# Kernel tuning notes

Hardware: AMD Instinct MI355X
Metric: run time of the kernel (lower is better)

The kernel has to match this reference:

```python
import jax, jax.numpy as jnp
import numpy as np

B = 1048576
INPUT_DIM = 64
NUM_LAYERS = 8   # number of trees
DEPTH = 6
TREE_DIM = 2
NUM_LEAVES = 2 ** DEPTH


def setup_inputs() -> dict:
    key = jax.random.key(0)
    ks = jax.random.split(key, 6)
    x = jax.random.normal(ks[0], (B, INPUT_DIM), dtype=jnp.float32)
    # Stacked per-tree, per-level Linear(input_dim, 1) selectors.
    W_sel = jax.random.normal(ks[1], (NUM_LAYERS, DEPTH, INPUT_DIM), dtype=jnp.float32) / np.sqrt(INPUT_DIM)
    b_sel = jax.random.normal(ks[2], (NUM_LAYERS, DEPTH), dtype=jnp.float32) * 0.01
    leaf_values = jax.random.normal(ks[3], (NUM_LAYERS, NUM_LEAVES, TREE_DIM), dtype=jnp.float32)
    fc_w = jax.random.normal(ks[4], (2, NUM_LAYERS * TREE_DIM), dtype=jnp.float32) / np.sqrt(NUM_LAYERS * TREE_DIM)
    fc_b = jax.random.normal(ks[5], (2,), dtype=jnp.float32) * 0.01
    return {"x": x, "W_sel": W_sel, "b_sel": b_sel, "leaf_values": leaf_values,
            "fc_w": fc_w, "fc_b": fc_b}


def reference(x, W_sel, b_sel, leaf_values, fc_w, fc_b):
    # All trees / levels in one contraction: [B, T, D]
    logits = jnp.einsum('bi,tdi->btd', x, W_sel) + b_sel
    # sigmoid(z) > 0.5  <=>  z > 0, but keep explicit sigmoid for faithfulness
    bits = (jax.nn.sigmoid(logits) > 0.5).astype(jnp.int32)  # [B, T, D]
    # leaf_indices = fold(idx*2 + bit) == sum bit_l * 2^(D-1-l)
    powers = (2 ** jnp.arange(DEPTH - 1, -1, -1)).astype(jnp.int32)  # [D]
    leaf_idx = jnp.sum(bits * powers, axis=-1)  # [B, T]
    # Per-tree leaf gather: leaf_values[t, leaf_idx[b, t]] -> [B, T, C]
    tree_ids = jnp.arange(NUM_LAYERS)[None, :]  # [1, T]
    leaves = leaf_values[tree_ids, leaf_idx]    # [B, T, C]
    concatenated = leaves.reshape(x.shape[0], NUM_LAYERS * TREE_DIM)
    return concatenated @ fc_w.T + fc_b
```

## Files before the change

kernel.cpp:

```cpp
#include <hip/hip_runtime.h>
#include <stdint.h>


typedef float f32x2 __attribute__((ext_vector_type(2)));
typedef float f32x4 __attribute__((ext_vector_type(4)));

static constexpr int   kBlocks = 4096;
static constexpr float kTau    = 1.5f * 0x1p-24f;
static constexpr float kMargin = 1e-4f;

__device__ __noinline__ float np_exact_dot(const float* __restrict__ xs,
                                           const float* __restrict__ w) {
#pragma clang fp contract(off)
  float s[4];
#pragma unroll
  for (int L = 0; L < 4; ++L) {
    float t = xs[12 + L] * w[12 + L];
    t = xs[8 + L] * w[8 + L] + t;
    t = xs[4 + L] * w[4 + L] + t;
    t = xs[0 + L] * w[0 + L] + t;
#pragma unroll
    for (int j = 1; j < 4; ++j) {
      const int o = 16 * j;
      t = xs[o + 12 + L] * w[o + 12 + L] + t;
      t = xs[o +  8 + L] * w[o +  8 + L] + t;
      t = xs[o +  4 + L] * w[o +  4 + L] + t;
      t = xs[o +  0 + L] * w[o +  0 + L] + t;
    }
    s[L] = t;
  }
  return (s[0] + s[1]) + (s[2] + s[3]);
}

__global__ __launch_bounds__(256) void forest_fast(
    const float* __restrict__ x,
    const float* __restrict__ Wsel,
    const float* __restrict__ bsel,
    const float* __restrict__ leaf,
    const float* __restrict__ fcw,
    const float* __restrict__ fcb,
    float* __restrict__ out)
{
  __shared__ f32x2 lleaf[512];
  ((f32x4*)lleaf)[threadIdx.x] = ((const f32x4*)leaf)[threadIdx.x];
  __syncthreads();

  const int lane = threadIdx.x & 63;
  const int wave = threadIdx.x >> 6;
  const int row  = (blockIdx.x * 4 + wave) * 64 + lane;
  const float* __restrict__ xrow = x + (size_t)row * 64;

  f32x2 xr2[32];
  {
    const f32x4* xp = (const f32x4*)xrow;
#pragma unroll
    for (int q = 0; q < 16; ++q) {
      const f32x4 v = xp[q];
      f32x2 h0; h0.x = v.x; h0.y = v.y;
      f32x2 h1; h1.x = v.z; h1.y = v.w;
      xr2[2 * q]     = h0;
      xr2[2 * q + 1] = h1;
    }
  }

  uint64_t bits = 0, flag = 0;
#pragma unroll 4
  for (int d = 0; d < 48; ++d) {
    const f32x2* __restrict__ w2 = (const f32x2*)(Wsel + d * 64);
    f32x2 c0 = {0.f, 0.f}, c1 = {0.f, 0.f}, c2 = {0.f, 0.f}, c3 = {0.f, 0.f};
#pragma unroll
    for (int i = 0; i < 8; ++i) {
      c0 = __builtin_elementwise_fma(xr2[4 * i + 0], w2[4 * i + 0], c0);
      c1 = __builtin_elementwise_fma(xr2[4 * i + 1], w2[4 * i + 1], c1);
      c2 = __builtin_elementwise_fma(xr2[4 * i + 2], w2[4 * i + 2], c2);
      c3 = __builtin_elementwise_fma(xr2[4 * i + 3], w2[4 * i + 3], c3);
    }
    const f32x2 s = (c0 + c1) + (c2 + c3);
    const float z = (s.x + s.y) + bsel[d];
    bits |= (uint64_t)(z > kTau ? 1u : 0u) << d;
    flag |= (uint64_t)(__builtin_fabsf(z - kTau) < kMargin ? 1u : 0u) << d;
  }

  while (flag) {
    const int d = __builtin_ctzll(flag);
    flag &= flag - 1;
    const float z = np_exact_dot(xrow, Wsel + d * 64) + bsel[d];
    const uint64_t m = 1ull << d;
    bits = (z > kTau) ? (bits | m) : (bits & ~m);
  }

  float o0 = fcb[0], o1 = fcb[1];
#pragma unroll
  for (int t = 0; t < 8; ++t) {
    int idx = 0;
#pragma unroll
    for (int l = 0; l < 6; ++l)
      idx = idx * 2 + (int)((bits >> (t * 6 + l)) & 1u);
    const f32x2 lv = lleaf[t * 64 + idx];
    o0 = fmaf(lv.x, fcw[2 * t], o0);
    o0 = fmaf(lv.y, fcw[2 * t + 1], o0);
    o1 = fmaf(lv.x, fcw[16 + 2 * t], o1);
    o1 = fmaf(lv.y, fcw[16 + 2 * t + 1], o1);
  }
  f32x2 r; r.x = o0; r.y = o1;
  ((f32x2*)out)[row] = r;
}

extern "C" void kernel_launch(void* const* d_in, const int* in_sizes, int n_in,
                              void* d_out, int out_size, void* d_ws, size_t ws_size,
                              hipStream_t stream) {
  (void)in_sizes; (void)n_in; (void)out_size; (void)d_ws; (void)ws_size;
  forest_fast<<<kBlocks, 256, 0, stream>>>(
      (const float*)d_in[0],
      (const float*)d_in[1],
      (const float*)d_in[2],
      (const float*)d_in[3],
      (const float*)d_in[4],
      (const float*)d_in[5],
      (float*)d_out);
}
```

Baseline: 394.6 us.

## Compute selector logits with split-bf16 MFMA instead of scalar FP32 FMAs

Replaces the per-lane 48x64 FP32 dot-product loop with 16x16x32 bf16 MFMA tiles. Both x and W are split into hi/lo bf16 parts so three products approximate FP32 accuracy. Decision bits and near-threshold flags are scattered across lanes, so they are combined with shuffles and then owned by the row's lane. The wider margin sends more near-zero logits to the exact FP32 recheck, and the lower split precision risks more fallback work.

Result: faster. 374.3 us (-5.2%).

```diff
diff --git a/kernel.cpp b/kernel.cpp
--- a/kernel.cpp
+++ b/kernel.cpp
@@ -1,13 +1,15 @@
 #include <hip/hip_runtime.h>
+#include <hip/hip_bf16.h>
 #include <stdint.h>
 
 
 typedef float f32x2 __attribute__((ext_vector_type(2)));
 typedef float f32x4 __attribute__((ext_vector_type(4)));
+typedef short short8 __attribute__((ext_vector_type(8)));
 
-static constexpr int   kBlocks = 4096;
-static constexpr float kTau    = 1.5f * 0x1p-24f;
-static constexpr float kMargin = 1e-4f;
+static constexpr int   kBlocks  = 4096;
+static constexpr float kTau     = 1.5f * 0x1p-24f;
+static constexpr float kMarginB = 2e-3f;
 
 __device__ __noinline__ float np_exact_dot(const float* __restrict__ xs,
                                            const float* __restrict__ w) {
@@ -32,7 +34,16 @@
   return (s[0] + s[1]) + (s[2] + s[3]);
 }
 
-__global__ __launch_bounds__(256) void forest_fast(
+__device__ __forceinline__ short bf16_hi(float v, float& hf) {
+  const __hip_bfloat16 h = __float2bfloat16(v);
+  hf = __bfloat162float(h);
+  return __builtin_bit_cast(short, h);
+}
+__device__ __forceinline__ short bf16_rn(float v) {
+  return __builtin_bit_cast(short, __float2bfloat16(v));
+}
+
+__global__ __launch_bounds__(256) void forest_mfma(
     const float* __restrict__ x,
     const float* __restrict__ Wsel,
     const float* __restrict__ bsel,
@@ -47,40 +58,98 @@
 
   const int lane = threadIdx.x & 63;
   const int wave = threadIdx.x >> 6;
-  const int row  = (blockIdx.x * 4 + wave) * 64 + lane;
-  const float* __restrict__ xrow = x + (size_t)row * 64;
+  const int q    = lane >> 4;
+  const int r16  = lane & 15;
+  const int rowbase = (blockIdx.x * 4 + wave) * 64;
 
-  f32x2 xr2[32];
-  {
-    const f32x4* xp = (const f32x4*)xrow;
+  short8 whi[3][2], wlo[3][2];
 #pragma unroll
-    for (int q = 0; q < 16; ++q) {
-      const f32x4 v = xp[q];
-      f32x2 h0; h0.x = v.x; h0.y = v.y;
-      f32x2 h1; h1.x = v.z; h1.y = v.w;
-      xr2[2 * q]     = h0;
-      xr2[2 * q + 1] = h1;
+  for (int rt = 0; rt < 3; ++rt) {
+#pragma unroll
+    for (int kh = 0; kh < 2; ++kh) {
+      const float* wp = Wsel + (rt * 16 + r16) * 64 + kh * 32 + q * 8;
+      const f32x4 w0 = *(const f32x4*)wp;
+      const f32x4 w1 = *(const f32x4*)(wp + 4);
+      short8 hi, lo;
+#pragma unroll
+      for (int i = 0; i < 4; ++i) {
+        float hf;
+        short h = bf16_hi(w0[i], hf);
+        hi[i] = h;     lo[i]     = bf16_rn(w0[i] - hf);
+        h = bf16_hi(w1[i], hf);
+        hi[4 + i] = h; lo[4 + i] = bf16_rn(w1[i] - hf);
+      }
+      whi[rt][kh] = hi; wlo[rt][kh] = lo;
     }
   }
 
-  uint64_t bits = 0, flag = 0;
-#pragma unroll 4
-  for (int d = 0; d < 48; ++d) {
-    const f32x2* __restrict__ w2 = (const f32x2*)(Wsel + d * 64);
-    f32x2 c0 = {0.f, 0.f}, c1 = {0.f, 0.f}, c2 = {0.f, 0.f}, c3 = {0.f, 0.f};
+  f32x4 taub[3];
 #pragma unroll
-    for (int i = 0; i < 8; ++i) {
-      c0 = __builtin_elementwise_fma(xr2[4 * i + 0], w2[4 * i + 0], c0);
-      c1 = __builtin_elementwise_fma(xr2[4 * i + 1], w2[4 * i + 1], c1);
-      c2 = __builtin_elementwise_fma(xr2[4 * i + 2], w2[4 * i + 2], c2);
-      c3 = __builtin_elementwise_fma(xr2[4 * i + 3], w2[4 * i + 3], c3);
-    }
-    const f32x2 s = (c0 + c1) + (c2 + c3);
-    const float z = (s.x + s.y) + bsel[d];
-    bits |= (uint64_t)(z > kTau ? 1u : 0u) << d;
-    flag |= (uint64_t)(__builtin_fabsf(z - kTau) < kMargin ? 1u : 0u) << d;
+  for (int rt = 0; rt < 3; ++rt) {
+    const f32x4 bs = *(const f32x4*)(bsel + rt * 16 + q * 4);
+    f32x4 t;
+#pragma unroll
+    for (int i = 0; i < 4; ++i) t[i] = kTau - bs[i];
+    taub[rt] = t;
   }
 
+  const float* xw = x + (size_t)(rowbase + r16) * 64 + q * 8;
+  f32x4 a0 = *(const f32x4*)(xw);
+  f32x4 a1 = *(const f32x4*)(xw + 4);
+  f32x4 a2 = *(const f32x4*)(xw + 32);
+  f32x4 a3 = *(const f32x4*)(xw + 36);
+
+  uint64_t bits = 0, flag = 0;
+
+#pragma unroll
+  for (int ct = 0; ct < 4; ++ct) {
+    short8 xh0, xl0, xh1, xl1;
+#pragma unroll
+    for (int i = 0; i < 4; ++i) {
+      float hf;
+      short h = bf16_hi(a0[i], hf); xh0[i]     = h; xl0[i]     = bf16_rn(a0[i] - hf);
+      h = bf16_hi(a1[i], hf);       xh0[4 + i] = h; xl0[4 + i] = bf16_rn(a1[i] - hf);
+      h = bf16_hi(a2[i], hf);       xh1[i]     = h; xl1[i]     = bf16_rn(a2[i] - hf);
+      h = bf16_hi(a3[i], hf);       xh1[4 + i] = h; xl1[4 + i] = bf16_rn(a3[i] - hf);
+    }
+    if (ct < 3) {
+      const float* p = xw + (size_t)(ct + 1) * 16 * 64;
+      a0 = *(const f32x4*)(p);      a1 = *(const f32x4*)(p + 4);
+      a2 = *(const f32x4*)(p + 32); a3 = *(const f32x4*)(p + 36);
+    }
+
+    f32x4 acc[3];
+#pragma unroll
+    for (int rt = 0; rt < 3; ++rt) {
+      f32x4 c = {0.f, 0.f, 0.f, 0.f};
+      c = __builtin_amdgcn_mfma_f32_16x16x32_bf16(whi[rt][0], xh0, c, 0, 0, 0);
+      c = __builtin_amdgcn_mfma_f32_16x16x32_bf16(whi[rt][1], xh1, c, 0, 0, 0);
+      c = __builtin_amdgcn_mfma_f32_16x16x32_bf16(whi[rt][0], xl0, c, 0, 0, 0);
+      c = __builtin_amdgcn_mfma_f32_16x16x32_bf16(whi[rt][1], xl1, c, 0, 0, 0);
+      c = __builtin_amdgcn_mfma_f32_16x16x32_bf16(wlo[rt][0], xh0, c, 0, 0, 0);
+      c = __builtin_amdgcn_mfma_f32_16x16x32_bf16(wlo[rt][1], xh1, c, 0, 0, 0);
+      acc[rt] = c;
+    }
+
+    uint64_t pb = 0, pf = 0;
+#pragma unroll
+    for (int rt = 0; rt < 3; ++rt) {
+#pragma unroll
+      for (int i = 0; i < 4; ++i) {
+        const float t = acc[rt][i] - taub[rt][i];
+        const int d = rt * 16 + q * 4 + i;
+        pb |= (uint64_t)(t > 0.f ? 1u : 0u) << d;
+        pf |= (uint64_t)(__builtin_fabsf(t) < kMarginB ? 1u : 0u) << d;
+      }
+    }
+    pb |= __shfl_xor((unsigned long long)pb, 16);
+    pb |= __shfl_xor((unsigned long long)pb, 32);
+    pf |= __shfl_xor((unsigned long long)pf, 16);
+    pf |= __shfl_xor((unsigned long long)pf, 32);
+    if (ct == q) { bits = pb; flag = pf; }
+  }
+
+  const float* __restrict__ xrow = x + (size_t)(rowbase + lane) * 64;
   while (flag) {
     const int d = __builtin_ctzll(flag);
     flag &= flag - 1;
@@ -103,14 +172,14 @@
     o1 = fmaf(lv.y, fcw[16 + 2 * t + 1], o1);
   }
   f32x2 r; r.x = o0; r.y = o1;
-  ((f32x2*)out)[row] = r;
+  ((f32x2*)out)[rowbase + lane] = r;
 }
 
 extern "C" void kernel_launch(void* const* d_in, const int* in_sizes, int n_in,
                               void* d_out, int out_size, void* d_ws, size_t ws_size,
                               hipStream_t stream) {
   (void)in_sizes; (void)n_in; (void)out_size; (void)d_ws; (void)ws_size;
-  forest_fast<<<kBlocks, 256, 0, stream>>>(
+  forest_mfma<<<kBlocks, 256, 0, stream>>>(
       (const float*)d_in[0],
       (const float*)d_in[1],
       (const float*)d_in[2],
```
